# Performance work log

Hardware: AMD Instinct MI355X
Metric: run time of the kernel (lower is better)

The kernel has to match this reference:

```python
import jax, jax.numpy as jnp
import numpy as np

DISCRETE_SIZE = 4  # -> 2-bit packing path
HALF_WIDTH = (DISCRETE_SIZE - 1) / 2.0  # 1.5
OFFSET = (DISCRETE_SIZE - 1) % 2 / 2.0  # 0.5


def pack_2bit(q):
    # q: uint8 flat array, values in {0..3}, length divisible by 4
    q = q.reshape(-1, 4)
    packed = (q[:, 0] | (q[:, 1] << 2) | (q[:, 2] << 4) | (q[:, 3] << 6)).astype(jnp.uint8)
    return packed


def unpack_2bit(packed, n):
    # packed: uint8 [N/4]; returns float32 [n]
    q = jnp.stack([(packed >> s) & 3 for s in (0, 2, 4, 6)], axis=-1).reshape(-1)
    return q[:n].astype(jnp.float32)


def setup_inputs() -> dict:
    key = jax.random.key(0)
    k0, k1, k2 = jax.random.split(key, 3)
    B, S, TD, CD = 8, 2048, 4096, 1024
    x = jax.random.normal(k0, (B, S, TD), dtype=jnp.float32)
    W_in = jax.random.normal(k1, (CD, TD), dtype=jnp.float32) * 0.02
    b_in = jnp.zeros((CD,), dtype=jnp.float32)
    W_out = jax.random.normal(k2, (TD, CD), dtype=jnp.float32) * 0.02
    b_out = jnp.zeros((TD,), dtype=jnp.float32)
    return {"x": x, "W_in": W_in, "b_in": b_in, "W_out": W_out, "b_out": b_out}


def reference(x, W_in, b_in, W_out, b_out):
    B, S, TD = x.shape
    CD = W_in.shape[0]
    # encode: in_proj + robust_minmax
    h = jnp.einsum('bst,ct->bsc', x, W_in) + b_in  # [B,S,CD]
    mean = h.mean()
    std = jnp.std(h, ddof=1)  # torch.std is unbiased
    q_min = mean - 3.0 * std
    q_max = mean + 3.0 * std
    h_clipped = jnp.clip(h, q_min, q_max)
    h_norm = 2.0 * (h_clipped - q_min + 1e-4) / (q_max - q_min + 1e-4) - 1.0

    # compress: scalar quantize to {0..3} levels
    fx = h_norm.reshape(-1, CD)
    x_round = jnp.round(fx * HALF_WIDTH - OFFSET)
    fxq = (x_round + OFFSET) / HALF_WIDTH
    indices = jnp.round(fxq * HALF_WIDTH + HALF_WIDTH).astype(jnp.uint8)  # {0..3}

    # commitment loss: 1 - cos_sim(fx, stop_grad(fxq)) averaged over rows
    fxq_det = jax.lax.stop_gradient(fxq)
    dot = (fx * fxq_det).sum(-1)
    sim = dot / (jnp.linalg.norm(fx, axis=-1) * jnp.linalg.norm(fxq_det, axis=-1) + 1e-3)
    L_comm = (1.0 - sim).sum() / sim.shape[0]

    # bit-pack then unpack (codebook index store/load)
    packed = pack_2bit(indices)
    rec = unpack_2bit(packed, indices.size).reshape(-1, CD)
    flat_xq = (rec - HALF_WIDTH) / HALF_WIDTH

    # decode: out_proj
    out = jnp.einsum('bsc,tc->bst', flat_xq.reshape(B, S, CD), W_out) + b_out
    return out, L_comm
```

## Files before the change

kernel.cpp:

```cpp
#include <hip/hip_runtime.h>

typedef __attribute__((ext_vector_type(4))) float f32x4;
typedef __attribute__((ext_vector_type(8))) short bf16x8;
typedef __attribute__((ext_vector_type(4))) short s16x4;

static __device__ __forceinline__ unsigned short f2bf(float x) {
  union { float f; unsigned u; } v; v.f = x;
  unsigned r = v.u + 0x7fffu + ((v.u >> 16) & 1u);
  return (unsigned short)(r >> 16);
}

struct StatsF { float mean, qmin, qmax, den; };

__global__ void k_convert(const float* __restrict__ Wout, unsigned short* __restrict__ Wo16,
                          int nWout) {
  int i = blockIdx.x * blockDim.x + threadIdx.x;
  int stride = gridDim.x * blockDim.x;
  for (int j = i; j < nWout; j += stride) Wo16[j] = f2bf(Wout[j]);
}

__global__ __launch_bounds__(256) void k_einsum5(
    const float* __restrict__ x, const float* __restrict__ Win,
    const float* __restrict__ bin, float* __restrict__ H, int K, int CD) {
  __shared__ __align__(16) float xs[128][68];
  __shared__ __align__(16) float wsd[32][68];
  const int tid = threadIdx.x;
  const long row0 = (long)blockIdx.y * 128;
  const int col0 = blockIdx.x * 32;
  const int lane = tid & 63;
  const int wv = tid >> 6;
  const int rA = lane, rB = lane + 64;

  float LA[8][4], LB[8][4];
#pragma unroll
  for (int c = 0; c < 8; ++c)
#pragma unroll
    for (int j = 0; j < 4; ++j) { LA[c][j] = 0.0f; LB[c][j] = 0.0f; }

  for (int kt = 0; kt < K; kt += 64) {
    __syncthreads();
#pragma unroll
    for (int p = 0; p < 8; ++p) {
      int lin = p * 256 + tid;
      int r = lin >> 4;
      int kq = lin & 15;
      float4 v = *reinterpret_cast<const float4*>(&x[(row0 + r) * (long)K + kt + kq * 4]);
      *reinterpret_cast<float4*>(&xs[r][kq * 4]) = v;
    }
#pragma unroll
    for (int p = 0; p < 2; ++p) {
      int lin = p * 256 + tid;
      int c = lin >> 4;
      int kq = lin & 15;
      float4 v = *reinterpret_cast<const float4*>(&Win[(long)(col0 + c) * K + kt + kq * 4]);
      *reinterpret_cast<float4*>(&wsd[c][kq * 4]) = v;
    }
    __syncthreads();
#pragma unroll
    for (int b = 0; b < 4; ++b) {
      const int kb = b * 16;
      const float4 a0 = *reinterpret_cast<const float4*>(&xs[rA][kb + 0]);
      const float4 a1 = *reinterpret_cast<const float4*>(&xs[rA][kb + 4]);
      const float4 a2 = *reinterpret_cast<const float4*>(&xs[rA][kb + 8]);
      const float4 a3 = *reinterpret_cast<const float4*>(&xs[rA][kb + 12]);
      const float4 e0 = *reinterpret_cast<const float4*>(&xs[rB][kb + 0]);
      const float4 e1 = *reinterpret_cast<const float4*>(&xs[rB][kb + 4]);
      const float4 e2 = *reinterpret_cast<const float4*>(&xs[rB][kb + 8]);
      const float4 e3 = *reinterpret_cast<const float4*>(&xs[rB][kb + 12]);
#pragma unroll
      for (int c = 0; c < 8; ++c) {
        const float* wrp = &wsd[wv * 8 + c][kb];
        const float4 w0 = *reinterpret_cast<const float4*>(wrp);
        const float4 w1 = *reinterpret_cast<const float4*>(wrp + 4);
        const float4 w2 = *reinterpret_cast<const float4*>(wrp + 8);
        const float4 w3 = *reinterpret_cast<const float4*>(wrp + 12);
        LA[c][0] = __fadd_rn(LA[c][0], __fmul_rn(a3.x, w3.x));
        LA[c][1] = __fadd_rn(LA[c][1], __fmul_rn(a3.y, w3.y));
        LA[c][2] = __fadd_rn(LA[c][2], __fmul_rn(a3.z, w3.z));
        LA[c][3] = __fadd_rn(LA[c][3], __fmul_rn(a3.w, w3.w));
        LA[c][0] = __fadd_rn(LA[c][0], __fmul_rn(a2.x, w2.x));
        LA[c][1] = __fadd_rn(LA[c][1], __fmul_rn(a2.y, w2.y));
        LA[c][2] = __fadd_rn(LA[c][2], __fmul_rn(a2.z, w2.z));
        LA[c][3] = __fadd_rn(LA[c][3], __fmul_rn(a2.w, w2.w));
        LA[c][0] = __fadd_rn(LA[c][0], __fmul_rn(a1.x, w1.x));
        LA[c][1] = __fadd_rn(LA[c][1], __fmul_rn(a1.y, w1.y));
        LA[c][2] = __fadd_rn(LA[c][2], __fmul_rn(a1.z, w1.z));
        LA[c][3] = __fadd_rn(LA[c][3], __fmul_rn(a1.w, w1.w));
        LA[c][0] = __fadd_rn(LA[c][0], __fmul_rn(a0.x, w0.x));
        LA[c][1] = __fadd_rn(LA[c][1], __fmul_rn(a0.y, w0.y));
        LA[c][2] = __fadd_rn(LA[c][2], __fmul_rn(a0.z, w0.z));
        LA[c][3] = __fadd_rn(LA[c][3], __fmul_rn(a0.w, w0.w));
        LB[c][0] = __fadd_rn(LB[c][0], __fmul_rn(e3.x, w3.x));
        LB[c][1] = __fadd_rn(LB[c][1], __fmul_rn(e3.y, w3.y));
        LB[c][2] = __fadd_rn(LB[c][2], __fmul_rn(e3.z, w3.z));
        LB[c][3] = __fadd_rn(LB[c][3], __fmul_rn(e3.w, w3.w));
        LB[c][0] = __fadd_rn(LB[c][0], __fmul_rn(e2.x, w2.x));
        LB[c][1] = __fadd_rn(LB[c][1], __fmul_rn(e2.y, w2.y));
        LB[c][2] = __fadd_rn(LB[c][2], __fmul_rn(e2.z, w2.z));
        LB[c][3] = __fadd_rn(LB[c][3], __fmul_rn(e2.w, w2.w));
        LB[c][0] = __fadd_rn(LB[c][0], __fmul_rn(e1.x, w1.x));
        LB[c][1] = __fadd_rn(LB[c][1], __fmul_rn(e1.y, w1.y));
        LB[c][2] = __fadd_rn(LB[c][2], __fmul_rn(e1.z, w1.z));
        LB[c][3] = __fadd_rn(LB[c][3], __fmul_rn(e1.w, w1.w));
        LB[c][0] = __fadd_rn(LB[c][0], __fmul_rn(e0.x, w0.x));
        LB[c][1] = __fadd_rn(LB[c][1], __fmul_rn(e0.y, w0.y));
        LB[c][2] = __fadd_rn(LB[c][2], __fmul_rn(e0.z, w0.z));
        LB[c][3] = __fadd_rn(LB[c][3], __fmul_rn(e0.w, w0.w));
      }
    }
  }
  float outA[8], outB[8];
#pragma unroll
  for (int c = 0; c < 8; ++c) {
    float bv = bin[col0 + wv * 8 + c];
    float h01 = __fadd_rn(LA[c][0], LA[c][1]);
    float h23 = __fadd_rn(LA[c][2], LA[c][3]);
    outA[c] = __fadd_rn(__fadd_rn(h01, h23), bv);
    float g01 = __fadd_rn(LB[c][0], LB[c][1]);
    float g23 = __fadd_rn(LB[c][2], LB[c][3]);
    outB[c] = __fadd_rn(__fadd_rn(g01, g23), bv);
  }
  float* hpA = &H[(row0 + rA) * (long)CD + col0 + wv * 8];
  *reinterpret_cast<float4*>(hpA) = *reinterpret_cast<float4*>(&outA[0]);
  *reinterpret_cast<float4*>(hpA + 4) = *reinterpret_cast<float4*>(&outA[4]);
  float* hpB = &H[(row0 + rB) * (long)CD + col0 + wv * 8];
  *reinterpret_cast<float4*>(hpB) = *reinterpret_cast<float4*>(&outB[0]);
  *reinterpret_cast<float4*>(hpB + 4) = *reinterpret_cast<float4*>(&outB[4]);
}

__global__ void k_sum1(const float* __restrict__ H, long n, double* __restrict__ part) {
  __shared__ double s1[256];
  long i = (long)blockIdx.x * 256 + threadIdx.x;
  long stride = (long)gridDim.x * 256;
  double a = 0.0;
  for (; i < n; i += stride) a += (double)H[i];
  s1[threadIdx.x] = a;
  __syncthreads();
  for (int s = 128; s > 0; s >>= 1) {
    if ((int)threadIdx.x < s) s1[threadIdx.x] += s1[threadIdx.x + s];
    __syncthreads();
  }
  if (threadIdx.x == 0) part[blockIdx.x] = s1[0];
}

__global__ void k_statsA(const double* __restrict__ part, int nPart, float fn,
                         StatsF* __restrict__ st) {
  __shared__ double s1[256];
  int tid = threadIdx.x;
  double a = 0.0;
  for (int i = tid; i < nPart; i += 256) a += part[i];
  s1[tid] = a;
  __syncthreads();
  for (int s = 128; s > 0; s >>= 1) {
    if (tid < s) s1[tid] += s1[tid + s];
    __syncthreads();
  }
  if (tid == 0) {
    float Sf = (float)s1[0];
    st->mean = __fdiv_rn(Sf, fn);
  }
}

__global__ void k_sumsq(const float* __restrict__ H, long n, const StatsF* __restrict__ st,
                        double* __restrict__ part) {
  __shared__ double s1[256];
  const float mean = st->mean;
  long i = (long)blockIdx.x * 256 + threadIdx.x;
  long stride = (long)gridDim.x * 256;
  double a = 0.0;
  for (; i < n; i += stride) {
    float d = __fsub_rn(H[i], mean);
    a += (double)__fmul_rn(d, d);
  }
  s1[threadIdx.x] = a;
  __syncthreads();
  for (int s = 128; s > 0; s >>= 1) {
    if ((int)threadIdx.x < s) s1[threadIdx.x] += s1[threadIdx.x + s];
    __syncthreads();
  }
  if (threadIdx.x == 0) part[blockIdx.x] = s1[0];
}

__global__ void k_statsB(const double* __restrict__ part, int nPart, float fnm1,
                         StatsF* __restrict__ st) {
  __shared__ double s1[256];
  int tid = threadIdx.x;
  double a = 0.0;
  for (int i = tid; i < nPart; i += 256) a += part[i];
  s1[tid] = a;
  __syncthreads();
  for (int s = 128; s > 0; s >>= 1) {
    if (tid < s) s1[tid] += s1[tid + s];
    __syncthreads();
  }
  if (tid == 0) {
    float SSf = (float)s1[0];
    float var = __fdiv_rn(SSf, fnm1);
    float sd = __fsqrt_rn(var);
    float mean = st->mean;
    float t3 = __fmul_rn(3.0f, sd);
    float qmin = __fsub_rn(mean, t3);
    float qmax = __fadd_rn(mean, t3);
    st->qmin = qmin;
    st->qmax = qmax;
    st->den = __fadd_rn(__fsub_rn(qmax, qmin), 1e-4f);
  }
}

__global__ __launch_bounds__(256) void k_quant(
    const float* __restrict__ H, const StatsF* __restrict__ st,
    unsigned short* __restrict__ A2, double* __restrict__ sims1, int CD) {
  __shared__ double red[3][4];
  const int tid = threadIdx.x;
  const long row = blockIdx.x;
  const float qmin = st->qmin, qmax = st->qmax, den = st->den;
  const float* hr = H + row * (long)CD;
  double dot = 0.0, n1 = 0.0, n2 = 0.0;
#pragma unroll
  for (int q = 0; q < 4; ++q) {
    int c = tid + q * 256;
    float h = hr[c];
    float hc = fminf(fmaxf(h, qmin), qmax);
    float d1 = __fsub_rn(hc, qmin);
    float d2 = __fadd_rn(d1, 1e-4f);
    float d3 = __fmul_rn(2.0f, d2);
    float d4 = __fdiv_rn(d3, den);
    float fx = __fsub_rn(d4, 1.0f);
    float t = __fsub_rn(__fmul_rn(fx, 1.5f), 0.5f);
    float r = rintf(t);
    float fxq = __fdiv_rn(__fadd_rn(r, 0.5f), 1.5f);
    A2[row * (long)CD + c] = f2bf(r + 0.5f);
    dot += (double)fx * (double)fxq;
    n1 += (double)fx * (double)fx;
    n2 += (double)fxq * (double)fxq;
  }
  const int wv = tid >> 6, lane = tid & 63;
  for (int s = 32; s > 0; s >>= 1) {
    dot += __shfl_down(dot, s);
    n1 += __shfl_down(n1, s);
    n2 += __shfl_down(n2, s);
  }
  if (lane == 0) { red[0][wv] = dot; red[1][wv] = n1; red[2][wv] = n2; }
  __syncthreads();
  if (tid == 0) {
    double D = red[0][0] + red[0][1] + red[0][2] + red[0][3];
    double N1 = red[1][0] + red[1][1] + red[1][2] + red[1][3];
    double N2 = red[2][0] + red[2][1] + red[2][2] + red[2][3];
    double sim = D / (sqrt(N1) * sqrt(N2) + 1e-3);
    sims1[row] = 1.0 - sim;
  }
}

__global__ void k_lred(const double* __restrict__ sims1, int nrows,
                       float* __restrict__ Out, long pos) {
  __shared__ double s1[256];
  int tid = threadIdx.x;
  double a = 0.0;
  for (int i = tid; i < nrows; i += 256) a += sims1[i];
  s1[tid] = a;
  __syncthreads();
  for (int s = 128; s > 0; s >>= 1) {
    if (tid < s) s1[tid] += s1[tid + s];
    __syncthreads();
  }
  if (tid == 0) Out[pos] = (float)(s1[0] / (double)nrows);
}

__global__ __launch_bounds__(256, 2) void k_gemm2(
    const unsigned short* __restrict__ A2u, const unsigned short* __restrict__ Bw,
    const float* __restrict__ bias, float* __restrict__ Out, int K, int N) {
  __shared__ unsigned short sA[128 * 64];
  __shared__ unsigned short sB[128 * 64];
  const int tid = threadIdx.x;
  const int lane = tid & 63;
  const int wid = tid >> 6;
  const int wr = (wid >> 1) * 64, wc = (wid & 1) * 64;
  const long row0 = (long)blockIdx.y * 128;
  const int col0 = blockIdx.x * 128;
  const int srow = tid >> 4, scol = tid & 15;
  const int l15 = lane & 15, lg = lane >> 4;

  f32x4 acc[4][4];
#pragma unroll
  for (int m = 0; m < 4; ++m)
#pragma unroll
    for (int n = 0; n < 4; ++n) acc[m][n] = f32x4{0.f, 0.f, 0.f, 0.f};

  for (int kt = 0; kt < K; kt += 64) {
    __syncthreads();
#pragma unroll
    for (int p = 0; p < 8; ++p) {
      int r = p * 16 + srow;
      s16x4 av = *reinterpret_cast<const s16x4*>(&A2u[(row0 + r) * (long)K + kt + scol * 4]);
      s16x4 bv = *reinterpret_cast<const s16x4*>(&Bw[(col0 + r) * (long)K + kt + scol * 4]);
      int off = r * 128 + ((scol * 8) ^ ((r & 7) << 4));
      *reinterpret_cast<s16x4*>((char*)sA + off) = av;
      *reinterpret_cast<s16x4*>((char*)sB + off) = bv;
    }
    __syncthreads();
#pragma unroll
    for (int kk = 0; kk < 2; ++kk) {
      bf16x8 fa[4], fb[4];
#pragma unroll
      for (int m = 0; m < 4; ++m) {
        int r = wr + m * 16 + l15;
        int off = r * 128 + (((kk * 64) + lg * 16) ^ ((r & 7) << 4));
        fa[m] = *reinterpret_cast<const bf16x8*>((char*)sA + off);
      }
#pragma unroll
      for (int n = 0; n < 4; ++n) {
        int r = wc + n * 16 + l15;
        int off = r * 128 + (((kk * 64) + lg * 16) ^ ((r & 7) << 4));
        fb[n] = *reinterpret_cast<const bf16x8*>((char*)sB + off);
      }
#pragma unroll
      for (int m = 0; m < 4; ++m)
#pragma unroll
        for (int n = 0; n < 4; ++n)
          acc[m][n] = __builtin_amdgcn_mfma_f32_16x16x32_bf16(fa[m], fb[n], acc[m][n], 0, 0, 0);
    }
  }
  const float inv = 1.0f / 1.5f;
#pragma unroll
  for (int m = 0; m < 4; ++m)
#pragma unroll
    for (int n = 0; n < 4; ++n) {
      int colg = col0 + wc + n * 16 + l15;
      float bv = bias[colg];
#pragma unroll
      for (int j = 0; j < 4; ++j) {
        long rowg = row0 + wr + m * 16 + lg * 4 + j;
        Out[rowg * (long)N + colg] = acc[m][n][j] * inv + bv;
      }
    }
}

extern "C" void kernel_launch(void* const* d_in, const int* in_sizes, int n_in,
                              void* d_out, int out_size, void* d_ws, size_t ws_size,
                              hipStream_t stream) {
  const float* x = (const float*)d_in[0];
  const float* Win = (const float*)d_in[1];
  const float* bin = (const float*)d_in[2];
  const float* Wout = (const float*)d_in[3];
  const float* bout = (const float*)d_in[4];
  const int CD = in_sizes[2];
  const int TD = in_sizes[4];
  const long M = (long)in_sizes[0] / TD;
  const long NH = M * CD;

  char* ws = (char*)d_ws;
  size_t off = 0;
  float* H = (float*)(ws + off); off += (size_t)NH * 4;
  unsigned short* A2 = (unsigned short*)(ws + off); off += (size_t)NH * 2;
  unsigned short* Wo16 = (unsigned short*)(ws + off); off += (size_t)TD * CD * 2;
  double* part = (double*)(ws + off); off += 2048 * 8;
  StatsF* st = (StatsF*)(ws + off); off += 256;
  double* sims1 = (double*)(ws + off); off += (size_t)M * 8;

  k_convert<<<512, 256, 0, stream>>>(Wout, Wo16, TD * CD);

  dim3 g1(CD / 32, M / 128);
  k_einsum5<<<g1, 256, 0, stream>>>(x, Win, bin, H, TD, CD);

  k_sum1<<<2048, 256, 0, stream>>>(H, NH, part);
  k_statsA<<<1, 256, 0, stream>>>(part, 2048, (float)NH, st);
  k_sumsq<<<2048, 256, 0, stream>>>(H, NH, st, part);
  k_statsB<<<1, 256, 0, stream>>>(part, 2048, (float)(NH - 1), st);

  k_quant<<<M, 256, 0, stream>>>(H, st, A2, sims1, CD);
  k_lred<<<1, 256, 0, stream>>>(sims1, (int)M, (float*)d_out, M * (long)TD);

  dim3 g2(TD / 128, M / 128);
  k_gemm2<<<g2, 256, 0, stream>>>(A2, Wo16, bout, (float*)d_out, CD, TD);
}
```

Measured before the change: 2.574 ms.

## Double-buffer first GEMM tiles with direct global-to-LDS loads and XOR swizzle

Rewrites the fp32 in-projection GEMM so x and W_in tiles are loaded straight into LDS with global_load_lds, double-buffered so the next K-slice loads while the current one is computed. The K step drops from 64 to 32, padding is removed, and x rows use an XOR swizzle to avoid LDS bank conflicts without padding. The goal is to hide global memory latency and remove the register round trip on staging. It relies on the ordering of async LDS writes relative to the barrier, and it doubles the number of barrier iterations.

```diff
diff --git a/kernel.cpp b/kernel.cpp
--- a/kernel.cpp
+++ b/kernel.cpp
@@ -8,6 +8,12 @@
   union { float f; unsigned u; } v; v.f = x;
   unsigned r = v.u + 0x7fffu + ((v.u >> 16) & 1u);
   return (unsigned short)(r >> 16);
+}
+
+static __device__ __forceinline__ void gl_lds16(const float* g, float* l) {
+  __builtin_amdgcn_global_load_lds(
+      (const __attribute__((address_space(1))) void*)g,
+      (__attribute__((address_space(3))) void*)l, 16, 0, 0);
 }
 
 struct StatsF { float mean, qmin, qmax, den; };
@@ -19,17 +25,19 @@
   for (int j = i; j < nWout; j += stride) Wo16[j] = f2bf(Wout[j]);
 }
 
-__global__ __launch_bounds__(256) void k_einsum5(
+__global__ __launch_bounds__(256) void k_einsum7(
     const float* __restrict__ x, const float* __restrict__ Win,
     const float* __restrict__ bin, float* __restrict__ H, int K, int CD) {
-  __shared__ __align__(16) float xs[128][68];
-  __shared__ __align__(16) float wsd[32][68];
+  __shared__ __align__(16) float xb[2][128 * 32];
+  __shared__ __align__(16) float wb[2][32 * 32];
   const int tid = threadIdx.x;
   const long row0 = (long)blockIdx.y * 128;
   const int col0 = blockIdx.x * 32;
   const int lane = tid & 63;
   const int wv = tid >> 6;
-  const int rA = lane, rB = lane + 64;
+  const int l3 = lane >> 3;
+  const int lc = lane & 7;
+  const int swz = lc ^ (l3 & 7);
 
   float LA[8][4], LB[8][4];
 #pragma unroll
@@ -37,77 +45,80 @@
 #pragma unroll
     for (int j = 0; j < 4; ++j) { LA[c][j] = 0.0f; LB[c][j] = 0.0f; }
 
-  for (int kt = 0; kt < K; kt += 64) {
-    __syncthreads();
-#pragma unroll
-    for (int p = 0; p < 8; ++p) {
-      int lin = p * 256 + tid;
-      int r = lin >> 4;
-      int kq = lin & 15;
-      float4 v = *reinterpret_cast<const float4*>(&x[(row0 + r) * (long)K + kt + kq * 4]);
-      *reinterpret_cast<float4*>(&xs[r][kq * 4]) = v;
-    }
-#pragma unroll
-    for (int p = 0; p < 2; ++p) {
-      int lin = p * 256 + tid;
-      int c = lin >> 4;
-      int kq = lin & 15;
-      float4 v = *reinterpret_cast<const float4*>(&Win[(long)(col0 + c) * K + kt + kq * 4]);
-      *reinterpret_cast<float4*>(&wsd[c][kq * 4]) = v;
-    }
-    __syncthreads();
-#pragma unroll
-    for (int b = 0; b < 4; ++b) {
-      const int kb = b * 16;
-      const float4 a0 = *reinterpret_cast<const float4*>(&xs[rA][kb + 0]);
-      const float4 a1 = *reinterpret_cast<const float4*>(&xs[rA][kb + 4]);
-      const float4 a2 = *reinterpret_cast<const float4*>(&xs[rA][kb + 8]);
-      const float4 a3 = *reinterpret_cast<const float4*>(&xs[rA][kb + 12]);
-      const float4 e0 = *reinterpret_cast<const float4*>(&xs[rB][kb + 0]);
-      const float4 e1 = *reinterpret_cast<const float4*>(&xs[rB][kb + 4]);
-      const float4 e2 = *reinterpret_cast<const float4*>(&xs[rB][kb + 8]);
-      const float4 e3 = *reinterpret_cast<const float4*>(&xs[rB][kb + 12]);
+  const float* xsrc0 = x + (row0 + wv * 8 + l3) * (long)K + swz * 4;
+  const float* wsrc = Win + (long)(col0 + wv * 8 + l3) * K + lc * 4;
+  const long xrstep = 32L * K;
+
+#pragma unroll
+  for (int p = 0; p < 4; ++p)
+    gl_lds16(xsrc0 + p * xrstep, &xb[0][(p * 32 + wv * 8) * 32]);
+  gl_lds16(wsrc, &wb[0][(wv * 8) * 32]);
+
+  int cur = 0;
+  for (int kt = 0; kt < K; kt += 32) {
+    __syncthreads();
+    if (kt + 32 < K) {
+      const int nxt = cur ^ 1;
+      const int kn = kt + 32;
+#pragma unroll
+      for (int p = 0; p < 4; ++p)
+        gl_lds16(xsrc0 + p * xrstep + kn, &xb[nxt][(p * 32 + wv * 8) * 32]);
+      gl_lds16(wsrc + kn, &wb[nxt][(wv * 8) * 32]);
+    }
+    const float* xr = &xb[cur][0];
+    const float* wr0 = &wb[cur][0];
+#pragma unroll
+    for (int b = 0; b < 2; ++b) {
+      const int kb4 = b * 4;
+      float4 a[4], e[4];
+#pragma unroll
+      for (int j = 0; j < 4; ++j) {
+        const int pc = ((kb4 + j) ^ lc) * 4;
+        a[j] = *reinterpret_cast<const float4*>(xr + lane * 32 + pc);
+        e[j] = *reinterpret_cast<const float4*>(xr + (lane + 64) * 32 + pc);
+      }
 #pragma unroll
       for (int c = 0; c < 8; ++c) {
-        const float* wrp = &wsd[wv * 8 + c][kb];
+        const float* wrp = wr0 + (wv * 8 + c) * 32 + b * 16;
         const float4 w0 = *reinterpret_cast<const float4*>(wrp);
         const float4 w1 = *reinterpret_cast<const float4*>(wrp + 4);
         const float4 w2 = *reinterpret_cast<const float4*>(wrp + 8);
         const float4 w3 = *reinterpret_cast<const float4*>(wrp + 12);
-        LA[c][0] = __fadd_rn(LA[c][0], __fmul_rn(a3.x, w3.x));
-        LA[c][1] = __fadd_rn(LA[c][1], __fmul_rn(a3.y, w3.y));
-        LA[c][2] = __fadd_rn(LA[c][2], __fmul_rn(a3.z, w3.z));
-        LA[c][3] = __fadd_rn(LA[c][3], __fmul_rn(a3.w, w3.w));
-        LA[c][0] = __fadd_rn(LA[c][0], __fmul_rn(a2.x, w2.x));
-        LA[c][1] = __fadd_rn(LA[c][1], __fmul_rn(a2.y, w2.y));
-        LA[c][2] = __fadd_rn(LA[c][2], __fmul_rn(a2.z, w2.z));
-        LA[c][3] = __fadd_rn(LA[c][3], __fmul_rn(a2.w, w2.w));
-        LA[c][0] = __fadd_rn(LA[c][0], __fmul_rn(a1.x, w1.x));
-        LA[c][1] = __fadd_rn(LA[c][1], __fmul_rn(a1.y, w1.y));
-        LA[c][2] = __fadd_rn(LA[c][2], __fmul_rn(a1.z, w1.z));
-        LA[c][3] = __fadd_rn(LA[c][3], __fmul_rn(a1.w, w1.w));
-        LA[c][0] = __fadd_rn(LA[c][0], __fmul_rn(a0.x, w0.x));
-        LA[c][1] = __fadd_rn(LA[c][1], __fmul_rn(a0.y, w0.y));
-        LA[c][2] = __fadd_rn(LA[c][2], __fmul_rn(a0.z, w0.z));
-        LA[c][3] = __fadd_rn(LA[c][3], __fmul_rn(a0.w, w0.w));
-        LB[c][0] = __fadd_rn(LB[c][0], __fmul_rn(e3.x, w3.x));
-        LB[c][1] = __fadd_rn(LB[c][1], __fmul_rn(e3.y, w3.y));
-        LB[c][2] = __fadd_rn(LB[c][2], __fmul_rn(e3.z, w3.z));
-        LB[c][3] = __fadd_rn(LB[c][3], __fmul_rn(e3.w, w3.w));
-        LB[c][0] = __fadd_rn(LB[c][0], __fmul_rn(e2.x, w2.x));
-        LB[c][1] = __fadd_rn(LB[c][1], __fmul_rn(e2.y, w2.y));
-        LB[c][2] = __fadd_rn(LB[c][2], __fmul_rn(e2.z, w2.z));
-        LB[c][3] = __fadd_rn(LB[c][3], __fmul_rn(e2.w, w2.w));
-        LB[c][0] = __fadd_rn(LB[c][0], __fmul_rn(e1.x, w1.x));
-        LB[c][1] = __fadd_rn(LB[c][1], __fmul_rn(e1.y, w1.y));
-        LB[c][2] = __fadd_rn(LB[c][2], __fmul_rn(e1.z, w1.z));
-        LB[c][3] = __fadd_rn(LB[c][3], __fmul_rn(e1.w, w1.w));
-        LB[c][0] = __fadd_rn(LB[c][0], __fmul_rn(e0.x, w0.x));
-        LB[c][1] = __fadd_rn(LB[c][1], __fmul_rn(e0.y, w0.y));
-        LB[c][2] = __fadd_rn(LB[c][2], __fmul_rn(e0.z, w0.z));
-        LB[c][3] = __fadd_rn(LB[c][3], __fmul_rn(e0.w, w0.w));
-      }
-    }
+        LA[c][0] = __fadd_rn(LA[c][0], __fmul_rn(a[3].x, w3.x));
+        LA[c][1] = __fadd_rn(LA[c][1], __fmul_rn(a[3].y, w3.y));
+        LA[c][2] = __fadd_rn(LA[c][2], __fmul_rn(a[3].z, w3.z));
+        LA[c][3] = __fadd_rn(LA[c][3], __fmul_rn(a[3].w, w3.w));
+        LA[c][0] = __fadd_rn(LA[c][0], __fmul_rn(a[2].x, w2.x));
+        LA[c][1] = __fadd_rn(LA[c][1], __fmul_rn(a[2].y, w2.y));
+        LA[c][2] = __fadd_rn(LA[c][2], __fmul_rn(a[2].z, w2.z));
+        LA[c][3] = __fadd_rn(LA[c][3], __fmul_rn(a[2].w, w2.w));
+        LA[c][0] = __fadd_rn(LA[c][0], __fmul_rn(a[1].x, w1.x));
+        LA[c][1] = __fadd_rn(LA[c][1], __fmul_rn(a[1].y, w1.y));
+        LA[c][2] = __fadd_rn(LA[c][2], __fmul_rn(a[1].z, w1.z));
+        LA[c][3] = __fadd_rn(LA[c][3], __fmul_rn(a[1].w, w1.w));
+        LA[c][0] = __fadd_rn(LA[c][0], __fmul_rn(a[0].x, w0.x));
+        LA[c][1] = __fadd_rn(LA[c][1], __fmul_rn(a[0].y, w0.y));
+        LA[c][2] = __fadd_rn(LA[c][2], __fmul_rn(a[0].z, w0.z));
+        LA[c][3] = __fadd_rn(LA[c][3], __fmul_rn(a[0].w, w0.w));
+        LB[c][0] = __fadd_rn(LB[c][0], __fmul_rn(e[3].x, w3.x));
+        LB[c][1] = __fadd_rn(LB[c][1], __fmul_rn(e[3].y, w3.y));
+        LB[c][2] = __fadd_rn(LB[c][2], __fmul_rn(e[3].z, w3.z));
+        LB[c][3] = __fadd_rn(LB[c][3], __fmul_rn(e[3].w, w3.w));
+        LB[c][0] = __fadd_rn(LB[c][0], __fmul_rn(e[2].x, w2.x));
+        LB[c][1] = __fadd_rn(LB[c][1], __fmul_rn(e[2].y, w2.y));
+        LB[c][2] = __fadd_rn(LB[c][2], __fmul_rn(e[2].z, w2.z));
+        LB[c][3] = __fadd_rn(LB[c][3], __fmul_rn(e[2].w, w2.w));
+        LB[c][0] = __fadd_rn(LB[c][0], __fmul_rn(e[1].x, w1.x));
+        LB[c][1] = __fadd_rn(LB[c][1], __fmul_rn(e[1].y, w1.y));
+        LB[c][2] = __fadd_rn(LB[c][2], __fmul_rn(e[1].z, w1.z));
+        LB[c][3] = __fadd_rn(LB[c][3], __fmul_rn(e[1].w, w1.w));
+        LB[c][0] = __fadd_rn(LB[c][0], __fmul_rn(e[0].x, w0.x));
+        LB[c][1] = __fadd_rn(LB[c][1], __fmul_rn(e[0].y, w0.y));
+        LB[c][2] = __fadd_rn(LB[c][2], __fmul_rn(e[0].z, w0.z));
+        LB[c][3] = __fadd_rn(LB[c][3], __fmul_rn(e[0].w, w0.w));
+      }
+    }
+    cur ^= 1;
   }
   float outA[8], outB[8];
 #pragma unroll
@@ -120,10 +131,10 @@
     float g23 = __fadd_rn(LB[c][2], LB[c][3]);
     outB[c] = __fadd_rn(__fadd_rn(g01, g23), bv);
   }
-  float* hpA = &H[(row0 + rA) * (long)CD + col0 + wv * 8];
+  float* hpA = &H[(row0 + lane) * (long)CD + col0 + wv * 8];
   *reinterpret_cast<float4*>(hpA) = *reinterpret_cast<float4*>(&outA[0]);
   *reinterpret_cast<float4*>(hpA + 4) = *reinterpret_cast<float4*>(&outA[4]);
-  float* hpB = &H[(row0 + rB) * (long)CD + col0 + wv * 8];
+  float* hpB = &H[(row0 + lane + 64) * (long)CD + col0 + wv * 8];
   *reinterpret_cast<float4*>(hpB) = *reinterpret_cast<float4*>(&outB[0]);
   *reinterpret_cast<float4*>(hpB + 4) = *reinterpret_cast<float4*>(&outB[4]);
 }
@@ -360,7 +371,7 @@
   k_convert<<<512, 256, 0, stream>>>(Wout, Wo16, TD * CD);
 
   dim3 g1(CD / 32, M / 128);
-  k_einsum5<<<g1, 256, 0, stream>>>(x, Win, bin, H, TD, CD);
+  k_einsum7<<<g1, 256, 0, stream>>>(x, Win, bin, H, TD, CD);
 
   k_sum1<<<2048, 256, 0, stream>>>(H, NH, part);
   k_statsA<<<1, 256, 0, stream>>>(part, 2048, (float)NH, st);
```

After: 2.795 ms. 1.09x slower.

## Double-buffer W_in tiles via direct global-to-LDS loads in first GEMM

Applied to the files above, without the earlier changes.

The W_in tile in the fp32 input-projection GEMM is now fetched with global_load_lds, which copies straight into LDS without going through registers, into two alternating buffers. The next k-step's weights are prefetched while the current step computes. The unpadded 64-wide LDS layout may add bank conflicts. No explicit vmcnt wait is visible before the buffer is read, so correctness depends on the barrier ordering.

```diff
diff --git a/kernel.cpp b/kernel.cpp
--- a/kernel.cpp
+++ b/kernel.cpp
@@ -8,6 +8,12 @@
   union { float f; unsigned u; } v; v.f = x;
   unsigned r = v.u + 0x7fffu + ((v.u >> 16) & 1u);
   return (unsigned short)(r >> 16);
+}
+
+static __device__ __forceinline__ void gl_lds16(const float* g, float* l) {
+  __builtin_amdgcn_global_load_lds(
+      (const __attribute__((address_space(1))) void*)g,
+      (__attribute__((address_space(3))) void*)l, 16, 0, 0);
 }
 
 struct StatsF { float mean, qmin, qmax, den; };
@@ -19,17 +25,18 @@
   for (int j = i; j < nWout; j += stride) Wo16[j] = f2bf(Wout[j]);
 }
 
-__global__ __launch_bounds__(256) void k_einsum5(
+__global__ __launch_bounds__(256) void k_einsum11(
     const float* __restrict__ x, const float* __restrict__ Win,
     const float* __restrict__ bin, float* __restrict__ H, int K, int CD) {
   __shared__ __align__(16) float xs[128][68];
-  __shared__ __align__(16) float wsd[32][68];
+  __shared__ __align__(16) float wb[2][32 * 64];
   const int tid = threadIdx.x;
   const long row0 = (long)blockIdx.y * 128;
   const int col0 = blockIdx.x * 32;
   const int lane = tid & 63;
   const int wv = tid >> 6;
   const int rA = lane, rB = lane + 64;
+  const int wl = lane;
 
   float LA[8][4], LB[8][4];
 #pragma unroll
@@ -37,6 +44,14 @@
 #pragma unroll
     for (int j = 0; j < 4; ++j) { LA[c][j] = 0.0f; LB[c][j] = 0.0f; }
 
+#pragma unroll
+  for (int p = 0; p < 2; ++p) {
+    int g = wv * 2 + p;
+    gl_lds16(&Win[(long)(col0 + g * 4 + (wl >> 4)) * K + (wl & 15) * 4],
+             &wb[0][g * 256]);
+  }
+
+  int cur = 0;
   for (int kt = 0; kt < K; kt += 64) {
     __syncthreads();
 #pragma unroll
@@ -47,15 +62,18 @@
       float4 v = *reinterpret_cast<const float4*>(&x[(row0 + r) * (long)K + kt + kq * 4]);
       *reinterpret_cast<float4*>(&xs[r][kq * 4]) = v;
     }
-#pragma unroll
-    for (int p = 0; p < 2; ++p) {
-      int lin = p * 256 + tid;
-      int c = lin >> 4;
-      int kq = lin & 15;
-      float4 v = *reinterpret_cast<const float4*>(&Win[(long)(col0 + c) * K + kt + kq * 4]);
-      *reinterpret_cast<float4*>(&wsd[c][kq * 4]) = v;
-    }
-    __syncthreads();
+    __syncthreads();
+    if (kt + 64 < K) {
+      const int nxt = cur ^ 1;
+      const int kn = kt + 64;
+#pragma unroll
+      for (int p = 0; p < 2; ++p) {
+        int g = wv * 2 + p;
+        gl_lds16(&Win[(long)(col0 + g * 4 + (wl >> 4)) * K + kn + (wl & 15) * 4],
+                 &wb[nxt][g * 256]);
+      }
+    }
+    const float* wcur = &wb[cur][0];
 #pragma unroll
     for (int b = 0; b < 4; ++b) {
       const int kb = b * 16;
@@ -69,7 +87,7 @@
       const float4 e3 = *reinterpret_cast<const float4*>(&xs[rB][kb + 12]);
 #pragma unroll
       for (int c = 0; c < 8; ++c) {
-        const float* wrp = &wsd[wv * 8 + c][kb];
+        const float* wrp = wcur + (wv * 8 + c) * 64 + kb;
         const float4 w0 = *reinterpret_cast<const float4*>(wrp);
         const float4 w1 = *reinterpret_cast<const float4*>(wrp + 4);
         const float4 w2 = *reinterpret_cast<const float4*>(wrp + 8);
@@ -108,6 +126,7 @@
         LB[c][3] = __fadd_rn(LB[c][3], __fmul_rn(e0.w, w0.w));
       }
     }
+    cur ^= 1;
   }
   float outA[8], outB[8];
 #pragma unroll
@@ -360,7 +379,7 @@
   k_convert<<<512, 256, 0, stream>>>(Wout, Wo16, TD * CD);
 
   dim3 g1(CD / 32, M / 128);
-  k_einsum5<<<g1, 256, 0, stream>>>(x, Win, bin, H, TD, CD);
+  k_einsum11<<<g1, 256, 0, stream>>>(x, Win, bin, H, TD, CD);
 
   k_sum1<<<2048, 256, 0, stream>>>(H, NH, part);
   k_statsA<<<1, 256, 0, stream>>>(part, 2048, (float)NH, st);
```

Result: slower. 4.209 ms (+63.5%).
